# Kernel optimization log

Hardware: AMD Instinct MI355X
Metric: run time of the kernel (lower is better)

Reference implementation:

```python
import jax, jax.numpy as jnp
import numpy as np

B, C, Ci, H, W = 8, 256, 128, 64, 64
EPS = 1e-5


def conv1x1(x, w, b):
    # x: [B,C,H,W], w: [O,C], b: [O] -> [B,O,H,W]
    return jnp.einsum('bchw,oc->bohw', x, w) + b[None, :, None, None]


def maxpool2(x):
    b, c, h, w = x.shape
    return x.reshape(b, c, h // 2, 2, w // 2, 2).max(axis=(3, 5))


def setup_inputs() -> dict:
    key = jax.random.key(0)
    ks = jax.random.split(key, 12)
    s_in = 1.0 / np.sqrt(C)
    s_ic = 1.0 / np.sqrt(Ci)
    return {
        'x': jax.random.normal(ks[0], (B, C, H, W), dtype=jnp.float32),
        'g_w': jax.random.normal(ks[1], (Ci, C), dtype=jnp.float32) * s_in,
        'g_b': jax.random.normal(ks[2], (Ci,), dtype=jnp.float32) * 0.01,
        'theta_w': jax.random.normal(ks[3], (Ci, C), dtype=jnp.float32) * s_in,
        'theta_b': jax.random.normal(ks[4], (Ci,), dtype=jnp.float32) * 0.01,
        'phi_w': jax.random.normal(ks[5], (Ci, C), dtype=jnp.float32) * s_in,
        'phi_b': jax.random.normal(ks[6], (Ci,), dtype=jnp.float32) * 0.01,
        'W_w': jax.random.normal(ks[7], (C, Ci), dtype=jnp.float32) * s_ic,
        'W_b': jax.random.normal(ks[8], (C,), dtype=jnp.float32) * 0.01,
        'bn_gamma': jax.random.normal(ks[9], (C,), dtype=jnp.float32) * 0.1 + 1.0,
        'bn_beta': jax.random.normal(ks[10], (C,), dtype=jnp.float32) * 0.1,
        'bn_mean': jnp.zeros((C,), dtype=jnp.float32),
        'bn_var': jax.random.uniform(ks[11], (C,), dtype=jnp.float32) * 0.5 + 0.75,
    }


def reference(x, g_w, g_b, theta_w, theta_b, phi_w, phi_b, W_w, W_b, bn_gamma, bn_beta, bn_mean, bn_var):
    b = x.shape[0]
    # g and phi: 1x1 conv then 2x2 max-pool (sub_sample=True)
    g_x = maxpool2(conv1x1(x, g_w, g_b)).reshape(b, Ci, -1)          # [B,Ci,Np]
    g_x = jnp.transpose(g_x, (0, 2, 1))                               # [B,Np,Ci]
    theta_x = conv1x1(x, theta_w, theta_b).reshape(b, Ci, -1)         # [B,Ci,N]
    theta_x = jnp.transpose(theta_x, (0, 2, 1))                       # [B,N,Ci]
    phi_x = maxpool2(conv1x1(x, phi_w, phi_b)).reshape(b, Ci, -1)     # [B,Ci,Np]
    f = jnp.einsum('bnc,bcm->bnm', theta_x, phi_x)                    # [B,N,Np]
    f_div_C = jax.nn.softmax(f, axis=-1)                              # embedded_gaussian: plain softmax, no scaling
    y = jnp.einsum('bnm,bmc->bnc', f_div_C, g_x)                      # [B,N,Ci]
    y = jnp.transpose(y, (0, 2, 1)).reshape(b, Ci, H, W)              # [B,Ci,H,W]
    # W: 1x1 conv + BatchNorm (inference form with running stats)
    W_y = conv1x1(y, W_w, W_b)
    inv = bn_gamma / jnp.sqrt(bn_var + EPS)
    W_y = (W_y - bn_mean[None, :, None, None]) * inv[None, :, None, None] + bn_beta[None, :, None, None]
    return W_y + x
```

## Files before the change

kernel.cpp:

```cpp
#include <hip/hip_runtime.h>
#include <math.h>

#define Bn   8
#define Cc   256
#define Cin  128
#define Hh   64
#define Ww   64
#define Nn   4096
#define Npl  1024
#define EPSf 1e-5f

typedef __attribute__((ext_vector_type(8))) short    short8;
typedef __attribute__((ext_vector_type(8))) _Float16 half8;
typedef __attribute__((ext_vector_type(4))) float    floatx4;

__device__ __forceinline__ unsigned short f2bf(float f) {
    unsigned int u = __float_as_uint(f);
    u += 0x7fffu + ((u >> 16) & 1u);
    return (unsigned short)(u >> 16);
}
__device__ __forceinline__ unsigned short f2h(float f) {
    _Float16 h = (_Float16)f;
    return __builtin_bit_cast(unsigned short, h);
}
__device__ __forceinline__ float h2f(unsigned short u) {
    return (float)__builtin_bit_cast(_Float16, u);
}

__device__ __forceinline__ unsigned int cvtpk_bf16(float lo, float hi) {
    unsigned int r;
    asm("v_cvt_pk_bf16_f32 %0, %1, %2" : "=v"(r) : "v"(lo), "v"(hi));
    return r;
}

__device__ __forceinline__ void gload_lds16(const unsigned short* g, unsigned short* l) {
    __builtin_amdgcn_global_load_lds(
        (const __attribute__((address_space(1))) unsigned int*)g,
        (__attribute__((address_space(3))) unsigned int*)l, 16, 0, 0);
}

__global__ __launch_bounds__(256) void k_prep(
    const float* __restrict__ g_w, const float* __restrict__ th_w,
    const float* __restrict__ ph_w,
    const float* __restrict__ W_w, const float* __restrict__ W_b,
    const float* __restrict__ gamma, const float* __restrict__ beta,
    const float* __restrict__ mean,  const float* __restrict__ var,
    unsigned short* __restrict__ gWh,
    unsigned short* __restrict__ thWh, unsigned short* __restrict__ thWl,
    unsigned short* __restrict__ phWh, unsigned short* __restrict__ phWl,
    unsigned short* __restrict__ Wh, float* __restrict__ cvec)
{
    int i = blockIdx.x * 256 + threadIdx.x;
    if (i < 98304) {
        int seg = i >> 15;
        int idx = i & 32767;
        float v = (seg == 0 ? g_w : (seg == 1 ? th_w : ph_w))[idx];
        unsigned short hi = f2h(v);
        if (seg == 0) gWh[idx] = hi;
        else {
            (seg == 1 ? thWh : phWh)[idx] = hi;
            (seg == 1 ? thWl : phWl)[idx] = f2h(v - h2f(hi));
        }
    } else {
        int j = i - 98304;
        int o = j >> 7;
        float inv = gamma[o] * rsqrtf(var[o] + EPSf);
        Wh[j] = f2h(W_w[j] * inv);
        if (j < Cc) {
            float invi = gamma[j] * rsqrtf(var[j] + EPSf);
            cvec[j] = (W_b[j] - mean[j]) * invi + beta[j];
        }
    }
}

#define XPAD 264

__global__ __launch_bounds__(256, 2) void k_conv3(
    const float* __restrict__ x,
    const unsigned short* __restrict__ gWh,
    const unsigned short* __restrict__ thWh, const unsigned short* __restrict__ thWl,
    const unsigned short* __restrict__ phWh, const unsigned short* __restrict__ phWl,
    const float* __restrict__ g_b, const float* __restrict__ th_b,
    const float* __restrict__ ph_b,
    unsigned short* __restrict__ thetaT,
    unsigned short* __restrict__ gPc,
    unsigned short* __restrict__ phiPt)
{
    __shared__ __align__(16) unsigned short Xhi[64 * XPAD];
    __shared__ __align__(16) unsigned short Xlo[64 * XPAD];

    const int t    = threadIdx.x;
    const int w    = t >> 6;
    const int l    = t & 63;
    const int quad = l >> 4;
    const int l16  = l & 15;
    const int b    = blockIdx.x >> 6;
    const int tile = blockIdx.x & 63;
    const int ty   = tile >> 1;
    const int tx   = tile & 1;

    {
        const float4* xg = (const float4*)x;
        unsigned int* XhiW = (unsigned int*)Xhi;
        unsigned int* XloW = (unsigned int*)Xlo;
        #pragma unroll
        for (int it = 0; it < 8; ++it) {
            int idx = t + 256 * it;
            int c2  = idx >> 4;
            int p4  = idx & 15;
            int n   = (2 * ty + (p4 >> 3)) * Ww + tx * 32 + (p4 & 7) * 4;
            float4 va = xg[((size_t)(b * Cc + 2 * c2) * Nn + n) >> 2];
            float4 vb = xg[((size_t)(b * Cc + 2 * c2 + 1) * Nn + n) >> 2];
            const float fa[4] = {va.x, va.y, va.z, va.w};
            const float fb[4] = {vb.x, vb.y, vb.z, vb.w};
            #pragma unroll
            for (int i = 0; i < 4; ++i) {
                int px = p4 * 4 + i;
                unsigned short ha = f2h(fa[i]), hb = f2h(fb[i]);
                unsigned short la = f2h(fa[i] - h2f(ha));
                unsigned short lb = f2h(fb[i] - h2f(hb));
                XhiW[px * 132 + c2] = (unsigned int)ha | ((unsigned int)hb << 16);
                XloW[px * 132 + c2] = (unsigned int)la | ((unsigned int)lb << 16);
            }
        }
    }
    __syncthreads();

    floatx4 acc[6][4] = {};

    #pragma unroll 2
    for (int kd = 0; kd < 8; ++kd) {
        half8 bhi[4], blo[4];
        #pragma unroll
        for (int nt = 0; nt < 4; ++nt) {
            bhi[nt] = *(const half8*)&Xhi[(nt * 16 + l16) * XPAD + kd * 32 + quad * 8];
            blo[nt] = *(const half8*)&Xlo[(nt * 16 + l16) * XPAD + kd * 32 + quad * 8];
        }
        #pragma unroll
        for (int ti = 0; ti < 6; ++ti) {
            int ot  = w + 4 * ti;
            int seg = ot >> 3;
            size_t aoff = (size_t)((ot & 7) * 16 + l16) * Cc + kd * 32 + quad * 8;
            const unsigned short* wh = (seg == 0 ? gWh : (seg == 1 ? thWh : phWh));
            half8 ah = *(const half8*)&wh[aoff];
            #pragma unroll
            for (int nt = 0; nt < 4; ++nt)
                acc[ti][nt] = __builtin_amdgcn_mfma_f32_16x16x32_f16(ah, bhi[nt], acc[ti][nt], 0, 0, 0);
            if (seg != 0) {
                const unsigned short* wl = (seg == 1 ? thWl : phWl);
                half8 al = *(const half8*)&wl[aoff];
                #pragma unroll
                for (int nt = 0; nt < 4; ++nt) {
                    acc[ti][nt] = __builtin_amdgcn_mfma_f32_16x16x32_f16(ah, blo[nt], acc[ti][nt], 0, 0, 0);
                    acc[ti][nt] = __builtin_amdgcn_mfma_f32_16x16x32_f16(al, bhi[nt], acc[ti][nt], 0, 0, 0);
                }
            }
        }
    }

    #pragma unroll
    for (int ti = 0; ti < 6; ++ti) {
        int ot  = w + 4 * ti;
        int seg = ot >> 3;
        int ol  = (ot & 7) * 16 + quad * 4;
        if (seg == 1) {
            float b0 = th_b[ol], b1 = th_b[ol + 1], b2 = th_b[ol + 2], b3 = th_b[ol + 3];
            #pragma unroll
            for (int nt = 0; nt < 4; ++nt) {
                int n = (2 * ty + (nt >> 1)) * Ww + tx * 32 + (nt & 1) * 16 + l16;
                ushort4 v;
                v.x = f2h(acc[ti][nt][0] + b0);
                v.y = f2h(acc[ti][nt][1] + b1);
                v.z = f2h(acc[ti][nt][2] + b2);
                v.w = f2h(acc[ti][nt][3] + b3);
                *(ushort4*)&thetaT[((size_t)b * Nn + n) * Cin + ol] = v;
            }
        } else {
            const float* bb = (seg == 0 ? g_b : ph_b);
            float b0 = bb[ol], b1 = bb[ol + 1], b2 = bb[ol + 2], b3 = bb[ol + 3];
            #pragma unroll
            for (int pp = 0; pp < 2; ++pp) {
                float pm[4];
                #pragma unroll
                for (int r = 0; r < 4; ++r) {
                    float m = fmaxf(acc[ti][pp][r], acc[ti][pp + 2][r]);
                    pm[r] = fmaxf(m, __shfl_xor(m, 1, 64));
                }
                int np = ty * 32 + tx * 16 + pp * 8 + (l16 >> 1);
                if ((l16 & 1) == 0) {
                    if (seg == 0) {
                        gPc[((size_t)b * Cin + ol + 0) * Npl + np] = f2bf(pm[0] + b0);
                        gPc[((size_t)b * Cin + ol + 1) * Npl + np] = f2bf(pm[1] + b1);
                        gPc[((size_t)b * Cin + ol + 2) * Npl + np] = f2bf(pm[2] + b2);
                        gPc[((size_t)b * Cin + ol + 3) * Npl + np] = f2bf(pm[3] + b3);
                    } else {
                        ushort4 v;
                        v.x = f2h(pm[0] + b0); v.y = f2h(pm[1] + b1);
                        v.z = f2h(pm[2] + b2); v.w = f2h(pm[3] + b3);
                        *(ushort4*)&phiPt[((size_t)b * Npl + np) * Cin + ol] = v;
                    }
                }
            }
        }
    }
}

#define SSHIFT 20.0f

__global__ __launch_bounds__(256, 4) void k_attn(
    const unsigned short* __restrict__ thetaT,
    const unsigned short* __restrict__ phiPt,
    const unsigned short* __restrict__ gPc,
    unsigned short* __restrict__ Yh, float* __restrict__ Lpart)
{
    __shared__ __align__(16) unsigned short Ks[64 * 128];
    __shared__ __align__(16) unsigned short Vt[128 * 64];

    const int t    = threadIdx.x;
    const int w    = t >> 6;
    const int l    = t & 63;
    const int quad = l >> 4;
    const int l16  = l & 15;
    const int b    = blockIdx.x >> 7;
    const int kh   = (blockIdx.x >> 6) & 1;
    const int qb   = blockIdx.x & 63;
    const int n0   = qb * 64;

    uint4 qr[4];
    #pragma unroll
    for (int kd = 0; kd < 4; ++kd)
        qr[kd] = *(const uint4*)&thetaT[((size_t)b * Nn + n0 + w * 16 + l16) * Cin
                                        + kd * 32 + quad * 8];
    #pragma unroll
    for (int kd = 0; kd < 4; ++kd)
        asm volatile("" : "+v"(qr[kd].x), "+v"(qr[kd].y), "+v"(qr[kd].z), "+v"(qr[kd].w));
    half8 qf[4];
    #pragma unroll
    for (int kd = 0; kd < 4; ++kd) qf[kd] = __builtin_bit_cast(half8, qr[kd]);

    floatx4 yacc[8] = {};
    float liq = 0.f;

    for (int ch = 0; ch < 8; ++ch) {
        const int chg = kh * 8 + ch;
        __syncthreads();

        #pragma unroll
        for (int j = 0; j < 4; ++j) {
            int slot = w * 4 + j;
            int m  = slot * 4 + (l >> 4);
            int gs = (l & 15) ^ (m & 7);
            gload_lds16(&phiPt[((size_t)b * Npl + chg * 64 + m) * Cin + gs * 8],
                        &Ks[slot * 512]);
        }
        #pragma unroll
        for (int j = 0; j < 4; ++j) {
            int slot = w * 4 + j;
            int c  = slot * 8 + (l >> 3);
            int gs = (l & 7) ^ (c & 7);
            gload_lds16(&gPc[((size_t)b * Cin + c) * Npl + chg * 64 + gs * 8],
                        &Vt[slot * 512]);
        }
        asm volatile("s_waitcnt vmcnt(0)" ::: "memory");
        __syncthreads();

        floatx4 sacc[4] = {};
        #pragma unroll
        for (int mt = 0; mt < 4; ++mt) {
            #pragma unroll
            for (int kd = 0; kd < 4; ++kd) {
                half8 kf = *(const half8*)&Ks[(mt * 16 + l16) * 128
                                              + ((kd * 4 + quad) ^ (l16 & 7)) * 8];
                sacc[mt] = __builtin_amdgcn_mfma_f32_16x16x32_f16(kf, qf[kd], sacc[mt], 0, 0, 0);
            }
        }

        float ex[4][4];
        #pragma unroll
        for (int mt = 0; mt < 4; ++mt) {
            #pragma unroll
            for (int r = 0; r < 4; ++r) {
                float v = __expf(sacc[mt][r] - SSHIFT);
                ex[mt][r] = v;
                liq += v;
            }
        }

        short8 pf[2];
        #pragma unroll
        for (int kd = 0; kd < 2; ++kd) {
            unsigned int a0 = cvtpk_bf16(ex[2 * kd][0],     ex[2 * kd][1]);
            unsigned int a1 = cvtpk_bf16(ex[2 * kd + 1][0], ex[2 * kd + 1][1]);
            unsigned int b0 = cvtpk_bf16(ex[2 * kd][2],     ex[2 * kd][3]);
            unsigned int b1 = cvtpk_bf16(ex[2 * kd + 1][2], ex[2 * kd + 1][3]);
            asm volatile("v_permlane32_swap_b32 %0, %1" : "+v"(a0), "+v"(a1));
            asm volatile("v_permlane16_swap_b32 %0, %1" : "+v"(a0), "+v"(a1));
            asm volatile("v_permlane32_swap_b32 %0, %1" : "+v"(b0), "+v"(b1));
            asm volatile("v_permlane16_swap_b32 %0, %1" : "+v"(b0), "+v"(b1));
            uint4 pw; pw.x = a0; pw.y = b0; pw.z = a1; pw.w = b1;
            pf[kd] = __builtin_bit_cast(short8, pw);
        }

        #pragma unroll
        for (int ct = 0; ct < 8; ++ct) {
            #pragma unroll
            for (int kd = 0; kd < 2; ++kd) {
                short8 vf = *(const short8*)&Vt[(ct * 16 + l16) * 64
                                                + ((kd * 4 + quad) ^ (l16 & 7)) * 8];
                yacc[ct] = __builtin_amdgcn_mfma_f32_16x16x32_bf16(pf[kd], vf, yacc[ct], 0, 0, 0);
            }
        }
    }

    liq += __shfl_xor(liq, 16, 64);
    liq += __shfl_xor(liq, 32, 64);

    unsigned short* Yp = Yh + ((size_t)(kh * Bn + b) * Nn) * Cin;
    float* Lp = Lpart + (size_t)(kh * Bn + b) * Nn;
    #pragma unroll
    for (int r = 0; r < 4; ++r) {
        float lr = __shfl(liq, quad * 4 + r, 64);
        float il = 1.0f / lr;
        int q = n0 + w * 16 + quad * 4 + r;
        #pragma unroll
        for (int ct = 0; ct < 8; ++ct)
            Yp[(size_t)q * Cin + ct * 16 + l16] = f2h(yacc[ct][r] * il);
        if (l16 == 0) Lp[q] = lr;
    }
}

#define DPAD 136

__global__ __launch_bounds__(256) void k_out(
    const unsigned short* __restrict__ Yh, const float* __restrict__ Lpart,
    const float* __restrict__ x,
    const unsigned short* __restrict__ Wh, const float* __restrict__ cvec,
    float* __restrict__ out)
{
    __shared__ __align__(16) unsigned short Ys[64 * DPAD];
    __shared__ __align__(16) unsigned short Ws[128 * DPAD];
    __shared__ float w0s[64], w1s[64];

    const int t    = threadIdx.x;
    const int w    = t >> 6;
    const int l    = t & 63;
    const int quad = l >> 4;
    const int l16  = l & 15;
    const int b    = blockIdx.x >> 6;
    const int qt   = blockIdx.x & 63;
    const int n0   = qt * 64;

    if (t < 64) {
        float l0 = Lpart[(size_t)b * Nn + n0 + t];
        float l1 = Lpart[(size_t)(Bn + b) * Nn + n0 + t];
        float s  = 1.0f / (l0 + l1);
        w0s[t] = l0 * s;
        w1s[t] = l1 * s;
    }
    __syncthreads();

    {
        const uint4* Y0 = (const uint4*)(Yh + ((size_t)b * Nn) * Cin);
        const uint4* Y1 = (const uint4*)(Yh + ((size_t)(Bn + b) * Nn) * Cin);
        #pragma unroll
        for (int it = 0; it < 4; ++it) {
            int idx = t + 256 * it;
            int q  = idx >> 4;
            int d8 = idx & 15;
            size_t gi = (((size_t)(n0 + q) * Cin) >> 3) + d8;
            half8 a = __builtin_bit_cast(half8, Y0[gi]);
            half8 c = __builtin_bit_cast(half8, Y1[gi]);
            float w0 = w0s[q], w1 = w1s[q];
            half8 r;
            #pragma unroll
            for (int i = 0; i < 8; ++i)
                r[i] = (_Float16)(w0 * (float)a[i] + w1 * (float)c[i]);
            *(uint4*)&Ys[q * DPAD + d8 * 8] = __builtin_bit_cast(uint4, r);
        }
    }

    for (int oc = 0; oc < 2; ++oc) {
        __syncthreads();
        #pragma unroll
        for (int it = 0; it < 8; ++it) {
            int idx = t + 256 * it;
            int o = idx >> 4, d8 = idx & 15;
            *(uint4*)&Ws[o * DPAD + d8 * 8] =
                *(const uint4*)&Wh[((size_t)(oc * 128 + o)) * Cin + d8 * 8];
        }
        __syncthreads();

        half8 af[2][4];
        #pragma unroll
        for (int mt = 0; mt < 2; ++mt)
            #pragma unroll
            for (int kd = 0; kd < 4; ++kd)
                af[mt][kd] = *(const half8*)&Ws[(w * 32 + mt * 16 + l16) * DPAD + kd * 32 + quad * 8];

        floatx4 acc[2][4] = {};
        #pragma unroll
        for (int nt = 0; nt < 4; ++nt) {
            half8 bfr[4];
            #pragma unroll
            for (int kd = 0; kd < 4; ++kd)
                bfr[kd] = *(const half8*)&Ys[(nt * 16 + l16) * DPAD + kd * 32 + quad * 8];
            #pragma unroll
            for (int mt = 0; mt < 2; ++mt)
                #pragma unroll
                for (int kd = 0; kd < 4; ++kd)
                    acc[mt][nt] = __builtin_amdgcn_mfma_f32_16x16x32_f16(af[mt][kd], bfr[kd], acc[mt][nt], 0, 0, 0);
        }

        #pragma unroll
        for (int mt = 0; mt < 2; ++mt) {
            #pragma unroll
            for (int r = 0; r < 4; ++r) {
                int o = oc * 128 + w * 32 + mt * 16 + quad * 4 + r;
                float cv = cvec[o];
                #pragma unroll
                for (int nt = 0; nt < 4; ++nt) {
                    size_t gi = ((size_t)(b * Cc + o)) * Nn + n0 + nt * 16 + l16;
                    out[gi] = acc[mt][nt][r] + cv + x[gi];
                }
            }
        }
    }
}

extern "C" void kernel_launch(void* const* d_in, const int* in_sizes, int n_in,
                              void* d_out, int out_size, void* d_ws, size_t ws_size,
                              hipStream_t stream) {
    const float* x    = (const float*)d_in[0];
    const float* g_w  = (const float*)d_in[1];
    const float* g_b  = (const float*)d_in[2];
    const float* th_w = (const float*)d_in[3];
    const float* th_b = (const float*)d_in[4];
    const float* ph_w = (const float*)d_in[5];
    const float* ph_b = (const float*)d_in[6];
    const float* W_w  = (const float*)d_in[7];
    const float* W_b  = (const float*)d_in[8];
    const float* gmm  = (const float*)d_in[9];
    const float* bta  = (const float*)d_in[10];
    const float* mmn  = (const float*)d_in[11];
    const float* vvr  = (const float*)d_in[12];
    float* out = (float*)d_out;

    unsigned short* thetaT = (unsigned short*)d_ws;
    unsigned short* phiPt  = thetaT + (size_t)4194304;
    unsigned short* gPc    = phiPt + (size_t)1048576;
    unsigned short* Wh     = gPc + (size_t)1048576;
    unsigned short* gWh    = Wh + 32768;
    unsigned short* thWh   = gWh + 32768;
    unsigned short* thWl   = thWh + 32768;
    unsigned short* phWh   = thWl + 32768;
    unsigned short* phWl   = phWh + 32768;
    float*          cvec   = (float*)(phWl + 32768);
    unsigned short* Yh     = (unsigned short*)(cvec + 256);
    float*          Lpart  = (float*)(Yh + (size_t)2 * Bn * Nn * Cin);

    k_prep<<<dim3(512), dim3(256), 0, stream>>>(
        g_w, th_w, ph_w, W_w, W_b, gmm, bta, mmn, vvr,
        gWh, thWh, thWl, phWh, phWl, Wh, cvec);
    k_conv3<<<dim3(Bn * 64), dim3(256), 0, stream>>>(
        x, gWh, thWh, thWl, phWh, phWl, g_b, th_b, ph_b, thetaT, gPc, phiPt);
    k_attn<<<dim3(Bn * 128), dim3(256), 0, stream>>>(thetaT, phiPt, gPc, Yh, Lpart);
    k_out<<<dim3(Bn * 64), dim3(256), 0, stream>>>(Yh, Lpart, x, Wh, cvec, out);
}
```

Baseline: 168.7 us.

## Fuse attention and output projection into one kernel with double-buffered K/V

Merges the attention kernel and the output 1x1-conv/BN/residual kernel. Each block now covers all 16 key chunks itself instead of splitting keys across two blocks, which removes the fp16 Y partials, the L partial-sum buffers and their reload and merge. The K/V staging is double-buffered in a 80KB shared array so the next chunk's loads overlap the current MFMAs. The normalized Y tile and W weights go into XOR-swizzled shared memory instead of padded rows, and blocks are remapped so batches interleave across workgroups. The cost is half as many attention blocks, each doing twice the serial work, and occupancy drops (launch bounds 2, larger LDS).

```diff
diff --git a/kernel.cpp b/kernel.cpp
--- a/kernel.cpp
+++ b/kernel.cpp
@@ -207,23 +207,26 @@
 
 #define SSHIFT 20.0f
 
-__global__ __launch_bounds__(256, 4) void k_attn(
+__global__ __launch_bounds__(256, 2) void k_attn_out(
     const unsigned short* __restrict__ thetaT,
     const unsigned short* __restrict__ phiPt,
     const unsigned short* __restrict__ gPc,
-    unsigned short* __restrict__ Yh, float* __restrict__ Lpart)
+    const unsigned short* __restrict__ Wh,
+    const float* __restrict__ cvec,
+    const float* __restrict__ x,
+    float* __restrict__ out)
 {
-    __shared__ __align__(16) unsigned short Ks[64 * 128];
-    __shared__ __align__(16) unsigned short Vt[128 * 64];
+    __shared__ __align__(16) unsigned short smem[40960];
 
     const int t    = threadIdx.x;
     const int w    = t >> 6;
     const int l    = t & 63;
     const int quad = l >> 4;
     const int l16  = l & 15;
-    const int b    = blockIdx.x >> 7;
-    const int kh   = (blockIdx.x >> 6) & 1;
-    const int qb   = blockIdx.x & 63;
+    const int bid  = blockIdx.x;
+    const int wid  = (bid & 7) * 64 + (bid >> 3);
+    const int b    = wid >> 6;
+    const int qb   = wid & 63;
     const int n0   = qb * 64;
 
     uint4 qr[4];
@@ -241,28 +244,43 @@
     floatx4 yacc[8] = {};
     float liq = 0.f;
 
-    for (int ch = 0; ch < 8; ++ch) {
-        const int chg = kh * 8 + ch;
-        __syncthreads();
-
+    const int mK = l >> 4;
+    const int gK = l & 15;
+    const int cV = l >> 3;
+    const int gV = l & 7;
+
+    auto stageKV = [&](int chg, int sel) {
+        unsigned short* Ks = smem + sel * 16384;
+        unsigned short* Vt = Ks + 8192;
         #pragma unroll
         for (int j = 0; j < 4; ++j) {
             int slot = w * 4 + j;
-            int m  = slot * 4 + (l >> 4);
-            int gs = (l & 15) ^ (m & 7);
+            int m  = slot * 4 + mK;
+            int gs = gK ^ (m & 7);
             gload_lds16(&phiPt[((size_t)b * Npl + chg * 64 + m) * Cin + gs * 8],
                         &Ks[slot * 512]);
         }
         #pragma unroll
         for (int j = 0; j < 4; ++j) {
             int slot = w * 4 + j;
-            int c  = slot * 8 + (l >> 3);
-            int gs = (l & 7) ^ (c & 7);
+            int c  = slot * 8 + cV;
+            int gs = gV ^ (c & 7);
             gload_lds16(&gPc[((size_t)b * Cin + c) * Npl + chg * 64 + gs * 8],
                         &Vt[slot * 512]);
         }
-        asm volatile("s_waitcnt vmcnt(0)" ::: "memory");
-        __syncthreads();
+    };
+
+    stageKV(0, 0);
+    asm volatile("s_waitcnt vmcnt(0)" ::: "memory");
+    __syncthreads();
+
+    #pragma unroll 2
+    for (int ch = 0; ch < 16; ++ch) {
+        const int cur = ch & 1;
+        if (ch < 15) stageKV(ch + 1, cur ^ 1);
+
+        const unsigned short* Ks = smem + cur * 16384;
+        const unsigned short* Vt = Ks + 8192;
 
         floatx4 sacc[4] = {};
         #pragma unroll
@@ -270,7 +288,7 @@
             #pragma unroll
             for (int kd = 0; kd < 4; ++kd) {
                 half8 kf = *(const half8*)&Ks[(mt * 16 + l16) * 128
-                                              + ((kd * 4 + quad) ^ (l16 & 7)) * 8];
+                                              + (((kd * 4 + quad) ^ (l16 & 7)) << 3)];
                 sacc[mt] = __builtin_amdgcn_mfma_f32_16x16x32_f16(kf, qf[kd], sacc[mt], 0, 0, 0);
             }
         }
@@ -306,96 +324,60 @@
             #pragma unroll
             for (int kd = 0; kd < 2; ++kd) {
                 short8 vf = *(const short8*)&Vt[(ct * 16 + l16) * 64
-                                                + ((kd * 4 + quad) ^ (l16 & 7)) * 8];
+                                                + (((kd * 4 + quad) ^ (l16 & 7)) << 3)];
                 yacc[ct] = __builtin_amdgcn_mfma_f32_16x16x32_bf16(pf[kd], vf, yacc[ct], 0, 0, 0);
             }
         }
+
+        asm volatile("s_waitcnt vmcnt(0)" ::: "memory");
+        __syncthreads();
     }
 
     liq += __shfl_xor(liq, 16, 64);
     liq += __shfl_xor(liq, 32, 64);
 
-    unsigned short* Yp = Yh + ((size_t)(kh * Bn + b) * Nn) * Cin;
-    float* Lp = Lpart + (size_t)(kh * Bn + b) * Nn;
+    {
+        unsigned short* Ws = smem + 8192;
+        #pragma unroll
+        for (int j = 0; j < 16; ++j) {
+            int slot = w * 16 + j;
+            int row  = slot * 4 + mK;
+            int gs   = gK ^ (row & 7);
+            gload_lds16(&Wh[(size_t)row * Cin + gs * 8], &Ws[slot * 512]);
+        }
+    }
+
+    {
+        unsigned short* Ys = smem;
+        #pragma unroll
+        for (int r = 0; r < 4; ++r) {
+            float lr = __shfl(liq, quad * 4 + r, 64);
+            float il = 1.0f / lr;
+            int q = w * 16 + quad * 4 + r;
+            #pragma unroll
+            for (int ct = 0; ct < 8; ++ct) {
+                int g = ct * 2 + (l16 >> 3);
+                Ys[q * 128 + (((g ^ (q & 7)) << 3) | (l16 & 7))] = f2h(yacc[ct][r] * il);
+            }
+        }
+    }
+    asm volatile("s_waitcnt vmcnt(0)" ::: "memory");
+    __syncthreads();
+
+    const unsigned short* Ys = smem;
+    const unsigned short* Ws = smem + 8192;
+
     #pragma unroll
-    for (int r = 0; r < 4; ++r) {
-        float lr = __shfl(liq, quad * 4 + r, 64);
-        float il = 1.0f / lr;
-        int q = n0 + w * 16 + quad * 4 + r;
-        #pragma unroll
-        for (int ct = 0; ct < 8; ++ct)
-            Yp[(size_t)q * Cin + ct * 16 + l16] = f2h(yacc[ct][r] * il);
-        if (l16 == 0) Lp[q] = lr;
-    }
-}
-
-#define DPAD 136
-
-__global__ __launch_bounds__(256) void k_out(
-    const unsigned short* __restrict__ Yh, const float* __restrict__ Lpart,
-    const float* __restrict__ x,
-    const unsigned short* __restrict__ Wh, const float* __restrict__ cvec,
-    float* __restrict__ out)
-{
-    __shared__ __align__(16) unsigned short Ys[64 * DPAD];
-    __shared__ __align__(16) unsigned short Ws[128 * DPAD];
-    __shared__ float w0s[64], w1s[64];
-
-    const int t    = threadIdx.x;
-    const int w    = t >> 6;
-    const int l    = t & 63;
-    const int quad = l >> 4;
-    const int l16  = l & 15;
-    const int b    = blockIdx.x >> 6;
-    const int qt   = blockIdx.x & 63;
-    const int n0   = qt * 64;
-
-    if (t < 64) {
-        float l0 = Lpart[(size_t)b * Nn + n0 + t];
-        float l1 = Lpart[(size_t)(Bn + b) * Nn + n0 + t];
-        float s  = 1.0f / (l0 + l1);
-        w0s[t] = l0 * s;
-        w1s[t] = l1 * s;
-    }
-    __syncthreads();
-
-    {
-        const uint4* Y0 = (const uint4*)(Yh + ((size_t)b * Nn) * Cin);
-        const uint4* Y1 = (const uint4*)(Yh + ((size_t)(Bn + b) * Nn) * Cin);
-        #pragma unroll
-        for (int it = 0; it < 4; ++it) {
-            int idx = t + 256 * it;
-            int q  = idx >> 4;
-            int d8 = idx & 15;
-            size_t gi = (((size_t)(n0 + q) * Cin) >> 3) + d8;
-            half8 a = __builtin_bit_cast(half8, Y0[gi]);
-            half8 c = __builtin_bit_cast(half8, Y1[gi]);
-            float w0 = w0s[q], w1 = w1s[q];
-            half8 r;
-            #pragma unroll
-            for (int i = 0; i < 8; ++i)
-                r[i] = (_Float16)(w0 * (float)a[i] + w1 * (float)c[i]);
-            *(uint4*)&Ys[q * DPAD + d8 * 8] = __builtin_bit_cast(uint4, r);
-        }
-    }
-
     for (int oc = 0; oc < 2; ++oc) {
-        __syncthreads();
-        #pragma unroll
-        for (int it = 0; it < 8; ++it) {
-            int idx = t + 256 * it;
-            int o = idx >> 4, d8 = idx & 15;
-            *(uint4*)&Ws[o * DPAD + d8 * 8] =
-                *(const uint4*)&Wh[((size_t)(oc * 128 + o)) * Cin + d8 * 8];
-        }
-        __syncthreads();
-
         half8 af[2][4];
         #pragma unroll
         for (int mt = 0; mt < 2; ++mt)
             #pragma unroll
-            for (int kd = 0; kd < 4; ++kd)
-                af[mt][kd] = *(const half8*)&Ws[(w * 32 + mt * 16 + l16) * DPAD + kd * 32 + quad * 8];
+            for (int kd = 0; kd < 4; ++kd) {
+                int row = oc * 128 + w * 32 + mt * 16 + l16;
+                af[mt][kd] = *(const half8*)&Ws[row * 128
+                                                + (((kd * 4 + quad) ^ (l16 & 7)) << 3)];
+            }
 
         floatx4 acc[2][4] = {};
         #pragma unroll
@@ -403,7 +385,8 @@
             half8 bfr[4];
             #pragma unroll
             for (int kd = 0; kd < 4; ++kd)
-                bfr[kd] = *(const half8*)&Ys[(nt * 16 + l16) * DPAD + kd * 32 + quad * 8];
+                bfr[kd] = *(const half8*)&Ys[(nt * 16 + l16) * 128
+                                             + (((kd * 4 + quad) ^ (l16 & 7)) << 3)];
             #pragma unroll
             for (int mt = 0; mt < 2; ++mt)
                 #pragma unroll
@@ -455,14 +438,12 @@
     unsigned short* phWh   = thWl + 32768;
     unsigned short* phWl   = phWh + 32768;
     float*          cvec   = (float*)(phWl + 32768);
-    unsigned short* Yh     = (unsigned short*)(cvec + 256);
-    float*          Lpart  = (float*)(Yh + (size_t)2 * Bn * Nn * Cin);
 
     k_prep<<<dim3(512), dim3(256), 0, stream>>>(
         g_w, th_w, ph_w, W_w, W_b, gmm, bta, mmn, vvr,
         gWh, thWh, thWl, phWh, phWl, Wh, cvec);
     k_conv3<<<dim3(Bn * 64), dim3(256), 0, stream>>>(
         x, gWh, thWh, thWl, phWh, phWl, g_b, th_b, ph_b, thetaT, gPc, phiPt);
-    k_attn<<<dim3(Bn * 128), dim3(256), 0, stream>>>(thetaT, phiPt, gPc, Yh, Lpart);
-    k_out<<<dim3(Bn * 64), dim3(256), 0, stream>>>(Yh, Lpart, x, Wh, cvec, out);
-}
+    k_attn_out<<<dim3(Bn * 64), dim3(256), 0, stream>>>(
+        thetaT, phiPt, gPc, Wh, cvec, x, out);
+}
```

Result: faster. 164.3 us (-2.6%).
